# Optimization experiments

Hardware: AMD Instinct MI355X
Metric: run time of the kernel (lower is better)

## Reference

```python
import jax, jax.numpy as jnp
import numpy as np

B, T, H, W, C = 4, 16, 56, 56, 128
NH = 4                       # num heads
HD = C // NH                 # head dim = 32
WS = (2, 7, 7)               # window shape (divides T,H,W -> no padding/bounding)
SS = (1, 3, 3)               # shift shape
N = WS[0] * WS[1] * WS[2]    # 98 tokens per window
L = (T // WS[0]) * (H // WS[1]) * (W // WS[2])  # 512 windows per sample
M = (2 * WS[0] - 1) * (2 * WS[1] - 1) * (2 * WS[2] - 1)  # 507 rel-pos entries
SCALE = HD ** -0.5
MLP_H = 4 * C


def _window_partition(x):
    b = x.shape[0]
    x = x.reshape(b, T // WS[0], WS[0], H // WS[1], WS[1], W // WS[2], WS[2], C)
    return x.transpose(0, 1, 3, 5, 2, 4, 6, 7).reshape(-1, N, C)


def _window_unpartition(win, b):
    x = win.reshape(b, T // WS[0], H // WS[1], W // WS[2], WS[0], WS[1], WS[2], C)
    return x.transpose(0, 1, 4, 2, 5, 3, 6, 7).reshape(b, T, H, W, C)


def _compute_mask():
    img = np.zeros((1, T, H, W, 1), dtype=np.float32)
    cnt = 0
    for ts in (slice(0, -WS[0]), slice(-WS[0], -SS[0]), slice(-SS[0], None)):
        for hs in (slice(0, -WS[1]), slice(-WS[1], -SS[1]), slice(-SS[1], None)):
            for ws in (slice(0, -WS[2]), slice(-WS[2], -SS[2]), slice(-SS[2], None)):
                img[:, ts, hs, ws, :] = cnt
                cnt += 1
    x = img.reshape(1, T // WS[0], WS[0], H // WS[1], WS[1], W // WS[2], WS[2], 1)
    mw = x.transpose(0, 1, 3, 5, 2, 4, 6, 7).reshape(-1, N)  # [L, N]
    am = mw[:, None, :] - mw[:, :, None]
    return np.where(am != 0, np.float32(-100.0), np.float32(0.0))


def _rel_pos_idx():
    coords = np.stack(np.meshgrid(np.arange(WS[0]), np.arange(WS[1]), np.arange(WS[2]), indexing='ij'))
    rel = coords.reshape(3, -1, 1) - coords.reshape(3, 1, -1)
    rel[0] += WS[0] - 1; rel[1] += WS[1] - 1; rel[2] += WS[2] - 1
    rel[0] *= (2 * WS[1] - 1) * (2 * WS[2] - 1)
    rel[1] *= 2 * WS[2] - 1
    return rel.sum(0).astype(np.int32)  # [N, N]


def _ln(x, g, b, eps=1e-5):
    mu = jnp.mean(x, axis=-1, keepdims=True)
    var = jnp.var(x, axis=-1, keepdims=True)
    return (x - mu) * jax.lax.rsqrt(var + eps) * g + b


def setup_inputs() -> dict:
    key = jax.random.key(0)
    ks = jax.random.split(key, 8)
    s = 0.02
    return {
        'x': jax.random.normal(ks[0], (B, T, H, W, C), jnp.float32),
        'g1': jnp.ones((C,), jnp.float32), 'b1': jnp.zeros((C,), jnp.float32),
        'w_qkv': jax.random.normal(ks[1], (C, 3 * C), jnp.float32) * s,
        'b_qkv': jnp.zeros((3 * C,), jnp.float32),
        'rel_pos_embed': jax.random.normal(ks[2], (NH, M), jnp.float32) * s,
        'w_proj': jax.random.normal(ks[3], (C, C), jnp.float32) * s,
        'b_proj': jnp.zeros((C,), jnp.float32),
        'g2': jnp.ones((C,), jnp.float32), 'b2': jnp.zeros((C,), jnp.float32),
        'w_fc1': jax.random.normal(ks[4], (C, MLP_H), jnp.float32) * s,
        'b_fc1': jnp.zeros((MLP_H,), jnp.float32),
        'w_fc2': jax.random.normal(ks[5], (MLP_H, C), jnp.float32) * s,
        'b_fc2': jnp.zeros((C,), jnp.float32),
        'attn_mask': jnp.asarray(_compute_mask()),      # [L, N, N]
        'rel_pos_idx': jnp.asarray(_rel_pos_idx()),     # [N, N] int32
    }


def reference(x, g1, b1, w_qkv, b_qkv, rel_pos_embed, w_proj, b_proj,
              g2, b2, w_fc1, b_fc1, w_fc2, b_fc2, attn_mask, rel_pos_idx):
    shortcut = x
    xn = _ln(x, g1, b1)
    # cyclic shift (shifted-window branch)
    sx = jnp.roll(xn, shift=(-SS[0], -SS[1], -SS[2]), axis=(1, 2, 3))
    win = _window_partition(sx)                         # [B*L, N, C]
    Bw = win.shape[0]
    qkv = (win @ w_qkv + b_qkv).reshape(Bw, N, 3, NH, HD).transpose(2, 0, 3, 1, 4)
    q, k, v = qkv[0] * SCALE, qkv[1], qkv[2]            # [Bw, NH, N, HD]
    attn = jnp.einsum('bhnd,bhmd->bhnm', q, k)          # [Bw, NH, N, N]
    bias = rel_pos_embed[:, rel_pos_idx.reshape(-1)].reshape(NH, N, N)
    attn = attn + bias[None]
    attn = attn.reshape(Bw // L, L, NH, N, N) + attn_mask[None, :, None]
    attn = jax.nn.softmax(attn.reshape(Bw, NH, N, N), axis=-1)
    out = jnp.einsum('bhnm,bhmd->bhnd', attn, v).transpose(0, 2, 1, 3).reshape(Bw, N, C)
    out = out @ w_proj + b_proj
    sx = _window_unpartition(out, x.shape[0])
    x2 = jnp.roll(sx, shift=SS, axis=(1, 2, 3))         # reverse shift
    x = shortcut + x2
    h = _ln(x, g2, b2)
    h = jax.nn.gelu(h @ w_fc1 + b_fc1, approximate=False)
    return x + (h @ w_fc2 + b_fc2)
```

## Files before the change

### kernel.cpp

```cpp
#include <hip/hip_runtime.h>
#include <hip/hip_bf16.h>
#include <cstdint>
#include <cstddef>

using bf16 = __hip_bfloat16;
typedef __attribute__((ext_vector_type(8))) short s8v;
typedef __attribute__((ext_vector_type(4))) float f4v;
typedef __attribute__((ext_vector_type(4))) unsigned short u16x4;

#define TT 16
#define HH 56
#define WWD 56
#define CC 128
#define NTOK 98
#define NWIN 2048
#define TOKENS 200704
#define MLPH 512
#define SCALEQ 0.17677669529663689f
#define NELEM 25690112LL

#define WS_WPT 49152
#define WS_W1T 65536
#define WS_W2T 131072
#define WS_RPE 196608
#define WS_BYTES 397280

__device__ __forceinline__ float bfu(unsigned short u) {
    return __uint_as_float(((unsigned int)u) << 16);
}
__device__ __forceinline__ unsigned short f2bu(float f) {
    bf16 h = __float2bfloat16(f);
    return *reinterpret_cast<unsigned short*>(&h);
}

__device__ __forceinline__ bool disc_f32(const void* g) {
    return *(const unsigned int*)g == 0x3F800000u;
}

template<bool F32> __device__ __forceinline__ float ldg(const void* p, size_t i) {
    if constexpr (F32) return ((const float*)p)[i];
    else return bfu(((const unsigned short*)p)[i]);
}
template<bool F32> __device__ __forceinline__ void stg(void* p, size_t i, float v) {
    if constexpr (F32) ((float*)p)[i] = v;
    else ((unsigned short*)p)[i] = f2bu(v);
}
template<bool F32> __device__ __forceinline__ unsigned short ldraw(const void* p, size_t i) {
    if constexpr (F32) return f2bu(((const float*)p)[i]);
    else return ((const unsigned short*)p)[i];
}
__device__ __forceinline__ unsigned short ldraw_rt(bool f32, const void* p, size_t i) {
    return f32 ? f2bu(((const float*)p)[i]) : ((const unsigned short*)p)[i];
}

__device__ __forceinline__ size_t shifted_offset(int bid) {
    int bw = bid / NTOK, n = bid - bw * NTOK;
    int b = bw >> 9, lw = bw & 511;
    int tw = lw >> 6, hw = (lw >> 3) & 7, ww = lw & 7;
    int t0 = n / 49; int r = n - t0 * 49; int h0 = r / 7; int w0 = r - h0 * 7;
    int ts = (tw * 2 + t0 + 1) & 15;
    int hs = hw * 7 + h0 + 3; if (hs >= HH) hs -= HH;
    int ws = ww * 7 + w0 + 3; if (ws >= WWD) ws -= WWD;
    return (size_t)(((b * TT + ts) * HH + hs) * WWD + ws) * CC;
}

__global__ __launch_bounds__(256) void k_prep_rt(const void* __restrict__ wq,
                                                 const void* __restrict__ wp,
                                                 const void* __restrict__ w1,
                                                 const void* __restrict__ w2,
                                                 const void* __restrict__ rpe,
                                                 unsigned short* __restrict__ ws,
                                                 int f32i) {
    bool f32 = (f32i != 0);
    int bid = blockIdx.x, t = threadIdx.x;
    if (bid == 48) {
        for (int u = t; u < 2032; u += 256)
            ws[WS_RPE + u] = (u < 2028) ? ldraw_rt(f32, rpe, u) : (unsigned short)0;
        return;
    }
    const void* src; unsigned short* dst; int R, C, tr, tc;
    if (bid < 12)      { src = wq; dst = ws;          R = 128; C = 384; tr = bid / 6;        tc = bid % 6; }
    else if (bid < 16) { src = wp; dst = ws + WS_WPT; R = 128; C = 128; tr = (bid - 12) / 2; tc = (bid - 12) & 1; }
    else if (bid < 32) { src = w1; dst = ws + WS_W1T; R = 128; C = 512; tr = (bid - 16) / 8; tc = (bid - 16) & 7; }
    else               { src = w2; dst = ws + WS_W2T; R = 512; C = 128; tr = (bid - 32) / 2; tc = (bid - 32) & 1; }
    __shared__ unsigned short tile[64][65];
    int ty = t >> 6, tx = t & 63;
#pragma unroll
    for (int k = 0; k < 16; ++k) {
        int row = k * 4 + ty;
        tile[row][tx] = ldraw_rt(f32, src, (size_t)(tr * 64 + row) * C + tc * 64 + tx);
    }
    __syncthreads();
#pragma unroll
    for (int k = 0; k < 16; ++k) {
        int col = k * 4 + ty;
        dst[(size_t)(tc * 64 + col) * R + tr * 64 + tx] = tile[tx][col];
    }
}

template<bool F32>
__global__ __launch_bounds__(256) void k_prep(const void* __restrict__ wq,
                                              const void* __restrict__ wp,
                                              const void* __restrict__ w1,
                                              const void* __restrict__ w2,
                                              const void* __restrict__ rpe,
                                              unsigned short* __restrict__ ws,
                                              const void* __restrict__ disc) {
    if (disc_f32(disc) != F32) return;
    int bid = blockIdx.x, t = threadIdx.x;
    if (bid == 48) {
        for (int u = t; u < 2032; u += 256)
            ws[WS_RPE + u] = (u < 2028) ? ldraw<F32>(rpe, u) : (unsigned short)0;
        return;
    }
    const void* src; unsigned short* dst; int R, C, tr, tc;
    if (bid < 12)      { src = wq; dst = ws;          R = 128; C = 384; tr = bid / 6;        tc = bid % 6; }
    else if (bid < 16) { src = wp; dst = ws + WS_WPT; R = 128; C = 128; tr = (bid - 12) / 2; tc = (bid - 12) & 1; }
    else if (bid < 32) { src = w1; dst = ws + WS_W1T; R = 128; C = 512; tr = (bid - 16) / 8; tc = (bid - 16) & 7; }
    else               { src = w2; dst = ws + WS_W2T; R = 512; C = 128; tr = (bid - 32) / 2; tc = (bid - 32) & 1; }
    __shared__ unsigned short tile[64][65];
    int ty = t >> 6, tx = t & 63;
#pragma unroll
    for (int k = 0; k < 16; ++k) {
        int row = k * 4 + ty;
        tile[row][tx] = ldraw<F32>(src, (size_t)(tr * 64 + row) * C + tc * 64 + tx);
    }
    __syncthreads();
#pragma unroll
    for (int k = 0; k < 16; ++k) {
        int col = k * 4 + ty;
        dst[(size_t)(tc * 64 + col) * R + tr * 64 + tx] = tile[tx][col];
    }
}

template<bool F32, bool PREP>
__global__ __launch_bounds__(256) void k_attn(const void* __restrict__ x,
                                              const void* __restrict__ g1,
                                              const void* __restrict__ b1,
                                              void* __restrict__ buf,
                                              const unsigned short* __restrict__ wsW,
                                              const void* __restrict__ bq,
                                              const void* __restrict__ wqRaw,
                                              const void* __restrict__ rpeRaw) {
    if (disc_f32(g1) != F32) return;
    __shared__ __align__(16) char smem[27552];
    int* off_i            = (int*)smem;
    int* info             = (int*)(smem + 448);
    unsigned short* xw    = (unsigned short*)(smem + 896);
    unsigned short* rpeh  = (unsigned short*)(smem + 896);
    unsigned short* Qh    = (unsigned short*)(smem + 1920);
    unsigned short* Kh    = (unsigned short*)(smem + 9760);
    unsigned short* VT    = (unsigned short*)(smem + 17600);

    int bw = blockIdx.x, lw = bw & 511, t = threadIdx.x;
    int wv = t >> 6, ln = t & 63;
    int qd = ln >> 4, lm = ln & 15;
    unsigned short* Stw = Qh + wv * 16 * 40;

    if (t < 112) {
        if (t < 98) {
            off_i[t] = (int)shifted_offset(bw * NTOK + t);
            int t0 = t / 49, r = t - t0 * 49, h0 = r / 7, w0 = r - h0 * 7;
            int tw = lw >> 6, hw = (lw >> 3) & 7, ww = lw & 7;
            int rt = (tw < 7) ? 0 : (t0 == 0 ? 1 : 2);
            int rh = (hw < 7) ? 0 : (h0 < 4 ? 1 : 2);
            int rw = (ww < 7) ? 0 : (w0 < 4 ? 1 : 2);
            info[t] = (t0 * 169 + h0 * 13 + w0) | (((rt * 3 + rh) * 3 + rw) << 10);
        } else {
            info[t] = 0;
        }
    }
    __syncthreads();

    for (int i = wv; i < 98; i += 4) {
        size_t off = (size_t)off_i[i];
        float v0 = ldg<F32>(x, off + ln), v1 = ldg<F32>(x, off + 64 + ln);
        float sm = v0 + v1, ss = v0 * v0 + v1 * v1;
#pragma unroll
        for (int o = 32; o > 0; o >>= 1) { sm += __shfl_xor(sm, o); ss += __shfl_xor(ss, o); }
        float mu = sm * (1.f / CC);
        float rstd = rsqrtf(ss * (1.f / CC) - mu * mu + 1e-5f);
        xw[i * 136 + ln]      = f2bu((v0 - mu) * rstd * ldg<F32>(g1, ln) + ldg<F32>(b1, ln));
        xw[i * 136 + 64 + ln] = f2bu((v1 - mu) * rstd * ldg<F32>(g1, ln + 64) + ldg<F32>(b1, ln + 64));
    }
    __syncthreads();

    s8v aF[2][4];
#pragma unroll
    for (int mi = 0; mi < 2; ++mi) {
        int m = wv + 4 * mi;
        int arow = (m <= 6) ? (m * 16 + lm) : 97;
        if (arow > 97) arow = 97;
#pragma unroll
        for (int ks = 0; ks < 4; ++ks)
            aF[mi][ks] = *(const s8v*)(xw + arow * 136 + ks * 32 + qd * 8);
    }
    __syncthreads();

    for (int i = t; i < 32 * 38; i += 256) VT[(i / 38) * 136 + 98 + (i % 38)] = 0;

    for (int h = 0; h < 4; ++h) {
        for (int u = t; u < 507; u += 256) {
            if constexpr (PREP) rpeh[u] = wsW[WS_RPE + h * 507 + u];
            else                rpeh[u] = ldraw<F32>(rpeRaw, h * 507 + u);
        }
        for (int g = 0; g < 6; ++g) {
            int seg = g >> 1;
            int gcol = seg * CC + h * 32 + (g & 1) * 16 + lm;
            s8v bfr[4];
            if constexpr (PREP) {
                const unsigned short* wc = wsW + (size_t)gcol * 128;
#pragma unroll
                for (int ks = 0; ks < 4; ++ks) bfr[ks] = *(const s8v*)(wc + ks * 32 + qd * 8);
            } else {
#pragma unroll
                for (int ks = 0; ks < 4; ++ks)
#pragma unroll
                    for (int j = 0; j < 8; ++j)
                        bfr[ks][j] = (short)ldraw<F32>(wqRaw, (size_t)(ks * 32 + qd * 8 + j) * 384 + gcol);
            }
            float bias = ldg<F32>(bq, gcol);
#pragma unroll
            for (int mi = 0; mi < 2; ++mi) {
                int m = wv + 4 * mi;
                if (m > 6) break;
                f4v acc = {0.f, 0.f, 0.f, 0.f};
#pragma unroll
                for (int ks = 0; ks < 4; ++ks)
                    acc = __builtin_amdgcn_mfma_f32_16x16x32_bf16(aF[mi][ks], bfr[ks], acc, 0, 0, 0);
#pragma unroll
                for (int ii = 0; ii < 4; ++ii) {
                    int tok = m * 16 + qd * 4 + ii;
                    if (tok < 98) {
                        unsigned short val = f2bu(acc[ii] + bias);
                        int dim = (g & 1) * 16 + lm;
                        if (seg == 0)      Qh[tok * 40 + dim] = val;
                        else if (seg == 1) Kh[tok * 40 + dim] = val;
                        else               VT[dim * 136 + tok] = val;
                    }
                }
            }
        }
        __syncthreads();

        for (int m = wv; m <= 6; m += 4) {
            int aci[4], idi[4];
#pragma unroll
            for (int ii = 0; ii < 4; ++ii) {
                int iw = info[m * 16 + qd * 4 + ii];
                aci[ii] = (iw & 1023) + 253;
                idi[ii] = iw >> 10;
            }
            int qrow = m * 16 + lm; if (qrow > 97) qrow = 97;
            s8v qf = *(const s8v*)(Qh + qrow * 40 + qd * 8);
            float v[7][4];
#pragma unroll
            for (int n = 0; n < 7; ++n) {
                int krow = n * 16 + lm; if (krow > 97) krow = 97;
                const s8v* bp = (const s8v*)(Kh + krow * 40 + qd * 8);
                f4v acc = {0.f, 0.f, 0.f, 0.f};
                acc = __builtin_amdgcn_mfma_f32_16x16x32_bf16(qf, *bp, acc, 0, 0, 0);
                int cj = info[n * 16 + lm];
                int aj = cj & 1023, idj = cj >> 10;
#pragma unroll
                for (int ii = 0; ii < 4; ++ii) {
                    int ti = m * 16 + qd * 4 + ii, tj = n * 16 + lm;
                    float biasv = bfu(rpeh[aci[ii] - aj]);
                    float maskv = (idi[ii] == idj) ? 0.f : -100.f;
                    v[n][ii] = (ti < 98 && tj < 98)
                        ? acc[ii] * SCALEQ + biasv + maskv : -1e30f;
                }
            }
#pragma unroll
            for (int ii = 0; ii < 4; ++ii) {
                float mx = v[0][ii];
#pragma unroll
                for (int n = 1; n < 7; ++n) mx = fmaxf(mx, v[n][ii]);
#pragma unroll
                for (int o = 8; o > 0; o >>= 1) mx = fmaxf(mx, __shfl_xor(mx, o));
                float sum = 0.f;
#pragma unroll
                for (int n = 0; n < 7; ++n) { float e = __expf(v[n][ii] - mx); v[n][ii] = e; sum += e; }
#pragma unroll
                for (int o = 8; o > 0; o >>= 1) sum += __shfl_xor(sum, o);
                float inv = 1.f / sum;
#pragma unroll
                for (int n = 0; n < 7; ++n) v[n][ii] *= inv;
            }
            f4v a0 = {0.f, 0.f, 0.f, 0.f}, a1 = {0.f, 0.f, 0.f, 0.f};
#pragma unroll
            for (int pair = 0; pair < 4; ++pair) {
                int n0 = pair * 2, n1 = pair * 2 + 1;
#pragma unroll
                for (int ii = 0; ii < 4; ++ii) {
                    Stw[(qd * 4 + ii) * 40 + lm]      = f2bu(v[n0][ii]);
                    Stw[(qd * 4 + ii) * 40 + 16 + lm] = (n1 < 7) ? f2bu(v[n1][ii]) : (unsigned short)0;
                }
                asm volatile("s_waitcnt lgkmcnt(0)" ::: "memory");
                const s8v* pa = (const s8v*)(Stw + lm * 40 + qd * 8);
                const s8v* pb0 = (const s8v*)(VT + lm * 136 + pair * 32 + qd * 8);
                const s8v* pb1 = (const s8v*)(VT + (16 + lm) * 136 + pair * 32 + qd * 8);
                a0 = __builtin_amdgcn_mfma_f32_16x16x32_bf16(*pa, *pb0, a0, 0, 0, 0);
                a1 = __builtin_amdgcn_mfma_f32_16x16x32_bf16(*pa, *pb1, a1, 0, 0, 0);
            }
#pragma unroll
            for (int ii = 0; ii < 4; ++ii) {
                int tok = m * 16 + qd * 4 + ii;
                if (tok < 98) {
                    stg<F32>(buf, (size_t)off_i[tok] + h * 32 + lm, a0[ii]);
                    stg<F32>(buf, (size_t)off_i[tok] + h * 32 + 16 + lm, a1[ii]);
                }
            }
        }
        __syncthreads();
    }
}

template<bool F32, bool PREP>
__global__ __launch_bounds__(256, 2) void k_pm(void* __restrict__ buf,
                                               const void* __restrict__ x,
                                               const unsigned short* __restrict__ wsW,
                                               const void* __restrict__ bpj,
                                               const void* __restrict__ g2,
                                               const void* __restrict__ b2,
                                               const void* __restrict__ bb1,
                                               const void* __restrict__ bb2,
                                               const void* __restrict__ disc,
                                               const void* __restrict__ wpRaw,
                                               const void* __restrict__ w1Raw,
                                               const void* __restrict__ w2Raw) {
    if (disc_f32(disc) != F32) return;
    __shared__ __align__(16) char smem[68608];
    unsigned short* Abf = (unsigned short*)smem;
    float* A32          = (float*)(smem + 17408);
    unsigned short* Hs  = (unsigned short*)(smem + 51200);
    int t = threadIdx.x, wv = t >> 6, ln = t & 63;
    int qd = ln >> 4, lm = ln & 15;
    size_t base = (size_t)blockIdx.x * 64;

    if constexpr (F32) {
        const f4v* src = (const f4v*)((const float*)buf + base * CC);
        for (int i = t * 4; i < 64 * 128; i += 1024) {
            f4v v = src[i >> 2];
            int row = i >> 7, c = i & 127;
            u16x4 pk;
#pragma unroll
            for (int j = 0; j < 4; ++j) pk[j] = f2bu(v[j]);
            *(u16x4*)(&Abf[row * 136 + c]) = pk;
        }
    } else {
        const s8v* src = (const s8v*)((const unsigned short*)buf + base * CC);
        for (int i = t * 8; i < 64 * 128; i += 2048) {
            s8v v = src[i >> 3];
            int row = i >> 7, c = i & 127;
            *(s8v*)(&Abf[row * 136 + c]) = v;
        }
    }
    __syncthreads();

    {
        s8v wpF[2][4]; float biasp[2];
#pragma unroll
        for (int gg = 0; gg < 2; ++gg) {
            int col = (wv + 4 * gg) * 16 + lm;
            if constexpr (PREP) {
                const unsigned short* wc = wsW + WS_WPT + (size_t)col * 128;
#pragma unroll
                for (int ks = 0; ks < 4; ++ks) wpF[gg][ks] = *(const s8v*)(wc + ks * 32 + qd * 8);
            } else {
#pragma unroll
                for (int ks = 0; ks < 4; ++ks)
#pragma unroll
                    for (int j = 0; j < 8; ++j)
                        wpF[gg][ks][j] = (short)ldraw<F32>(wpRaw, (size_t)(ks * 32 + qd * 8 + j) * 128 + col);
            }
            biasp[gg] = ldg<F32>(bpj, col);
        }
#pragma unroll
        for (int m = 0; m < 4; ++m) {
            s8v aF[4];
#pragma unroll
            for (int ks = 0; ks < 4; ++ks)
                aF[ks] = *(const s8v*)(Abf + (m * 16 + lm) * 136 + ks * 32 + qd * 8);
#pragma unroll
            for (int gg = 0; gg < 2; ++gg) {
                int col = (wv + 4 * gg) * 16 + lm;
                f4v acc = {0.f, 0.f, 0.f, 0.f};
#pragma unroll
                for (int ks = 0; ks < 4; ++ks)
                    acc = __builtin_amdgcn_mfma_f32_16x16x32_bf16(aF[ks], wpF[gg][ks], acc, 0, 0, 0);
#pragma unroll
                for (int ii = 0; ii < 4; ++ii) {
                    int row = m * 16 + qd * 4 + ii;
                    A32[row * 132 + col] = acc[ii] + biasp[gg] + ldg<F32>(x, (base + row) * CC + col);
                }
            }
        }
    }
    __syncthreads();

#pragma unroll
    for (int r = 0; r < 16; ++r) {
        int row = wv + 4 * r;
        float v0 = A32[row * 132 + ln], v1 = A32[row * 132 + 64 + ln];
        float sm = v0 + v1, ss = v0 * v0 + v1 * v1;
#pragma unroll
        for (int o = 32; o > 0; o >>= 1) { sm += __shfl_xor(sm, o); ss += __shfl_xor(ss, o); }
        float mu = sm * (1.f / CC);
        float rstd = rsqrtf(ss * (1.f / CC) - mu * mu + 1e-5f);
        Abf[row * 136 + ln]      = f2bu((v0 - mu) * rstd * ldg<F32>(g2, ln) + ldg<F32>(b2, ln));
        Abf[row * 136 + 64 + ln] = f2bu((v1 - mu) * rstd * ldg<F32>(g2, ln + 64) + ldg<F32>(b2, ln + 64));
    }
    __syncthreads();

    s8v aFrag[4][4];
#pragma unroll
    for (int m = 0; m < 4; ++m)
#pragma unroll
        for (int ks = 0; ks < 4; ++ks)
            aFrag[m][ks] = *(const s8v*)(Abf + (m * 16 + lm) * 136 + ks * 32 + qd * 8);

    f4v acc2[2][4];
#pragma unroll
    for (int gg = 0; gg < 2; ++gg)
#pragma unroll
        for (int m = 0; m < 4; ++m) acc2[gg][m] = {0.f, 0.f, 0.f, 0.f};

    for (int q = 0; q < 4; ++q) {
#pragma unroll
        for (int gg = 0; gg < 2; ++gg) {
            int colL = (wv + 4 * gg) * 16 + lm;
            int colG = q * 128 + colL;
            s8v bfr[4];
            if constexpr (PREP) {
                const unsigned short* wc = wsW + WS_W1T + (size_t)colG * 128;
#pragma unroll
                for (int ks = 0; ks < 4; ++ks) bfr[ks] = *(const s8v*)(wc + ks * 32 + qd * 8);
            } else {
#pragma unroll
                for (int ks = 0; ks < 4; ++ks)
#pragma unroll
                    for (int j = 0; j < 8; ++j)
                        bfr[ks][j] = (short)ldraw<F32>(w1Raw, (size_t)(ks * 32 + qd * 8 + j) * MLPH + colG);
            }
            float bias = ldg<F32>(bb1, colG);
#pragma unroll
            for (int m = 0; m < 4; ++m) {
                f4v acc = {0.f, 0.f, 0.f, 0.f};
#pragma unroll
                for (int ks = 0; ks < 4; ++ks)
                    acc = __builtin_amdgcn_mfma_f32_16x16x32_bf16(aFrag[m][ks], bfr[ks], acc, 0, 0, 0);
#pragma unroll
                for (int ii = 0; ii < 4; ++ii) {
                    int row = m * 16 + qd * 4 + ii;
                    float hv = acc[ii] + bias;
                    Hs[row * 136 + colL] = f2bu(0.5f * hv * (1.f + erff(hv * 0.70710678118654752f)));
                }
            }
        }
        s8v w2f[2][4];
#pragma unroll
        for (int gg = 0; gg < 2; ++gg) {
            int col = (wv * 2 + gg) * 16 + lm;
            if constexpr (PREP) {
                const unsigned short* wc = wsW + WS_W2T + (size_t)col * 512 + q * 128;
#pragma unroll
                for (int ksl = 0; ksl < 4; ++ksl) w2f[gg][ksl] = *(const s8v*)(wc + ksl * 32 + qd * 8);
            } else {
#pragma unroll
                for (int ksl = 0; ksl < 4; ++ksl)
#pragma unroll
                    for (int j = 0; j < 8; ++j)
                        w2f[gg][ksl][j] = (short)ldraw<F32>(w2Raw, (size_t)(q * 128 + ksl * 32 + qd * 8 + j) * CC + col);
            }
        }
        __syncthreads();
#pragma unroll
        for (int m = 0; m < 4; ++m) {
            s8v hF[4];
#pragma unroll
            for (int ksl = 0; ksl < 4; ++ksl)
                hF[ksl] = *(const s8v*)(Hs + (m * 16 + lm) * 136 + ksl * 32 + qd * 8);
#pragma unroll
            for (int gg = 0; gg < 2; ++gg)
#pragma unroll
                for (int ksl = 0; ksl < 4; ++ksl)
                    acc2[gg][m] = __builtin_amdgcn_mfma_f32_16x16x32_bf16(hF[ksl], w2f[gg][ksl], acc2[gg][m], 0, 0, 0);
        }
        __syncthreads();
    }

#pragma unroll
    for (int gg = 0; gg < 2; ++gg) {
        int col = (wv * 2 + gg) * 16 + lm;
        float bias = ldg<F32>(bb2, col);
#pragma unroll
        for (int m = 0; m < 4; ++m) {
#pragma unroll
            for (int ii = 0; ii < 4; ++ii) {
                int row = m * 16 + qd * 4 + ii;
                stg<F32>(buf, (base + row) * CC + col,
                         acc2[gg][m][ii] + bias + A32[row * 132 + col]);
            }
        }
    }
}

extern "C" void kernel_launch(void* const* d_in, const int* in_sizes, int n_in,
                              void* d_out, int out_size, void* d_ws, size_t ws_size,
                              hipStream_t stream) {
    const void* x    = d_in[0];
    const void* g1   = d_in[1];
    const void* b1   = d_in[2];
    const void* wqkv = d_in[3];
    const void* bqkv = d_in[4];
    const void* rpe  = d_in[5];
    const void* wp   = d_in[6];
    const void* bp   = d_in[7];
    const void* g2   = d_in[8];
    const void* b2   = d_in[9];
    const void* w1   = d_in[10];
    const void* bb1  = d_in[11];
    const void* w2   = d_in[12];
    const void* bb2  = d_in[13];
    void* buf = d_out;
    unsigned short* wsW = (unsigned short*)d_ws;

    bool use_ws = (d_ws != nullptr) && (ws_size >= (size_t)WS_BYTES);

    long long xb = (long long)in_sizes[0];
    bool known_f32  = (xb == NELEM * 4);
    bool known_bf16 = (xb == NELEM * 2);

    if (use_ws && (known_f32 || known_bf16)) {
        k_prep_rt<<<49, 256, 0, stream>>>(wqkv, wp, w1, w2, rpe, wsW, known_f32 ? 1 : 0);
        if (known_f32) {
            k_attn<true, true><<<NWIN, 256, 0, stream>>>(x, g1, b1, buf, wsW, bqkv, wqkv, rpe);
            k_pm<true, true><<<TOKENS / 64, 256, 0, stream>>>(buf, x, wsW, bp, g2, b2, bb1, bb2, g1, wp, w1, w2);
        } else {
            k_attn<false, true><<<NWIN, 256, 0, stream>>>(x, g1, b1, buf, wsW, bqkv, wqkv, rpe);
            k_pm<false, true><<<TOKENS / 64, 256, 0, stream>>>(buf, x, wsW, bp, g2, b2, bb1, bb2, g1, wp, w1, w2);
        }
        return;
    }

    if (use_ws) {
        k_prep<false><<<49, 256, 0, stream>>>(wqkv, wp, w1, w2, rpe, wsW, g1);
        k_prep<true> <<<49, 256, 0, stream>>>(wqkv, wp, w1, w2, rpe, wsW, g1);
        k_attn<false, true><<<NWIN, 256, 0, stream>>>(x, g1, b1, buf, wsW, bqkv, wqkv, rpe);
        k_attn<true,  true><<<NWIN, 256, 0, stream>>>(x, g1, b1, buf, wsW, bqkv, wqkv, rpe);
        k_pm<false, true><<<TOKENS / 64, 256, 0, stream>>>(buf, x, wsW, bp, g2, b2, bb1, bb2, g1, wp, w1, w2);
        k_pm<true,  true><<<TOKENS / 64, 256, 0, stream>>>(buf, x, wsW, bp, g2, b2, bb1, bb2, g1, wp, w1, w2);
    } else if (known_f32 || known_bf16) {
        if (known_f32) {
            k_attn<true, false><<<NWIN, 256, 0, stream>>>(x, g1, b1, buf, wsW, bqkv, wqkv, rpe);
            k_pm<true, false><<<TOKENS / 64, 256, 0, stream>>>(buf, x, wsW, bp, g2, b2, bb1, bb2, g1, wp, w1, w2);
        } else {
            k_attn<false, false><<<NWIN, 256, 0, stream>>>(x, g1, b1, buf, wsW, bqkv, wqkv, rpe);
            k_pm<false, false><<<TOKENS / 64, 256, 0, stream>>>(buf, x, wsW, bp, g2, b2, bb1, bb2, g1, wp, w1, w2);
        }
    } else {
        k_attn<false, false><<<NWIN, 256, 0, stream>>>(x, g1, b1, buf, wsW, bqkv, wqkv, rpe);
        k_attn<true,  false><<<NWIN, 256, 0, stream>>>(x, g1, b1, buf, wsW, bqkv, wqkv, rpe);
        k_pm<false, false><<<TOKENS / 64, 256, 0, stream>>>(buf, x, wsW, bp, g2, b2, bb1, bb2, g1, wp, w1, w2);
        k_pm<true,  false><<<TOKENS / 64, 256, 0, stream>>>(buf, x, wsW, bp, g2, b2, bb1, bb2, g1, wp, w1, w2);
    }
}
```

Baseline: 569.4 us.

## Prefetch next fc1 weight chunk and stage residual x into LDS with input

The residual x tile is now loaded in the same coalesced vectorized pass as the attention output and written straight into the fp32 LDS buffer. This replaces the scattered per-element global reads of x in the projection epilogue. The fc1 weight fragments for the next 128-column chunk are prefetched into registers before the barrier, so their load latency overlaps the fc2 MFMA work, and the loop is fully unrolled. The cost is higher register pressure from the double-buffered weight fragments, which may lower occupancy.

```diff
diff --git a/kernel.cpp b/kernel.cpp
--- a/kernel.cpp
+++ b/kernel.cpp
@@ -339,21 +339,34 @@
     size_t base = (size_t)blockIdx.x * 64;
 
     if constexpr (F32) {
-        const f4v* src = (const f4v*)((const float*)buf + base * CC);
+        const f4v* srcb = (const f4v*)((const float*)buf + base * CC);
+        const f4v* srcx = (const f4v*)((const float*)x + base * CC);
         for (int i = t * 4; i < 64 * 128; i += 1024) {
-            f4v v = src[i >> 2];
+            f4v v = srcb[i >> 2];
+            f4v xv = srcx[i >> 2];
             int row = i >> 7, c = i & 127;
             u16x4 pk;
 #pragma unroll
             for (int j = 0; j < 4; ++j) pk[j] = f2bu(v[j]);
             *(u16x4*)(&Abf[row * 136 + c]) = pk;
+            *(f4v*)(&A32[row * 132 + c]) = xv;
         }
     } else {
-        const s8v* src = (const s8v*)((const unsigned short*)buf + base * CC);
+        const s8v* srcb = (const s8v*)((const unsigned short*)buf + base * CC);
+        const s8v* srcx = (const s8v*)((const unsigned short*)x + base * CC);
         for (int i = t * 8; i < 64 * 128; i += 2048) {
-            s8v v = src[i >> 3];
+            s8v v = srcb[i >> 3];
+            s8v xv = srcx[i >> 3];
             int row = i >> 7, c = i & 127;
             *(s8v*)(&Abf[row * 136 + c]) = v;
+            f4v x0, x1;
+#pragma unroll
+            for (int j = 0; j < 4; ++j) {
+                x0[j] = bfu((unsigned short)xv[j]);
+                x1[j] = bfu((unsigned short)xv[j + 4]);
+            }
+            *(f4v*)(&A32[row * 132 + c])     = x0;
+            *(f4v*)(&A32[row * 132 + c + 4]) = x1;
         }
     }
     __syncthreads();
@@ -392,7 +405,7 @@
 #pragma unroll
                 for (int ii = 0; ii < 4; ++ii) {
                     int row = m * 16 + qd * 4 + ii;
-                    A32[row * 132 + col] = acc[ii] + biasp[gg] + ldg<F32>(x, (base + row) * CC + col);
+                    A32[row * 132 + col] += acc[ii] + biasp[gg];
                 }
             }
         }
@@ -426,34 +439,48 @@
 #pragma unroll
         for (int m = 0; m < 4; ++m) acc2[gg][m] = {0.f, 0.f, 0.f, 0.f};
 
+#define LOADW1(Q, W, B)                                                          \
+    {                                                                            \
+        _Pragma("unroll")                                                        \
+        for (int gg = 0; gg < 2; ++gg) {                                         \
+            int colL = (wv + 4 * gg) * 16 + lm;                                  \
+            int colG = (Q) * 128 + colL;                                         \
+            if constexpr (PREP) {                                                \
+                const unsigned short* wc = wsW + WS_W1T + (size_t)colG * 128;    \
+                _Pragma("unroll")                                                \
+                for (int ks = 0; ks < 4; ++ks)                                   \
+                    W[gg][ks] = *(const s8v*)(wc + ks * 32 + qd * 8);            \
+            } else {                                                             \
+                _Pragma("unroll")                                                \
+                for (int ks = 0; ks < 4; ++ks)                                   \
+                    _Pragma("unroll")                                            \
+                    for (int j = 0; j < 8; ++j)                                  \
+                        W[gg][ks][j] = (short)ldraw<F32>(w1Raw,                  \
+                            (size_t)(ks * 32 + qd * 8 + j) * MLPH + colG);       \
+            }                                                                    \
+            B[gg] = ldg<F32>(bb1, colG);                                         \
+        }                                                                        \
+    }
+
+    s8v w1A[2][4], w1B[2][4];
+    float b1A[2], b1B[2];
+    LOADW1(0, w1A, b1A);
+
+#pragma unroll
     for (int q = 0; q < 4; ++q) {
 #pragma unroll
         for (int gg = 0; gg < 2; ++gg) {
             int colL = (wv + 4 * gg) * 16 + lm;
-            int colG = q * 128 + colL;
-            s8v bfr[4];
-            if constexpr (PREP) {
-                const unsigned short* wc = wsW + WS_W1T + (size_t)colG * 128;
-#pragma unroll
-                for (int ks = 0; ks < 4; ++ks) bfr[ks] = *(const s8v*)(wc + ks * 32 + qd * 8);
-            } else {
-#pragma unroll
-                for (int ks = 0; ks < 4; ++ks)
-#pragma unroll
-                    for (int j = 0; j < 8; ++j)
-                        bfr[ks][j] = (short)ldraw<F32>(w1Raw, (size_t)(ks * 32 + qd * 8 + j) * MLPH + colG);
-            }
-            float bias = ldg<F32>(bb1, colG);
 #pragma unroll
             for (int m = 0; m < 4; ++m) {
                 f4v acc = {0.f, 0.f, 0.f, 0.f};
 #pragma unroll
                 for (int ks = 0; ks < 4; ++ks)
-                    acc = __builtin_amdgcn_mfma_f32_16x16x32_bf16(aFrag[m][ks], bfr[ks], acc, 0, 0, 0);
+                    acc = __builtin_amdgcn_mfma_f32_16x16x32_bf16(aFrag[m][ks], w1A[gg][ks], acc, 0, 0, 0);
 #pragma unroll
                 for (int ii = 0; ii < 4; ++ii) {
                     int row = m * 16 + qd * 4 + ii;
-                    float hv = acc[ii] + bias;
+                    float hv = acc[ii] + b1A[gg];
                     Hs[row * 136 + colL] = f2bu(0.5f * hv * (1.f + erff(hv * 0.70710678118654752f)));
                 }
             }
@@ -474,6 +501,7 @@
                         w2f[gg][ksl][j] = (short)ldraw<F32>(w2Raw, (size_t)(q * 128 + ksl * 32 + qd * 8 + j) * CC + col);
             }
         }
+        if (q < 3) LOADW1(q + 1, w1B, b1B);
         __syncthreads();
 #pragma unroll
         for (int m = 0; m < 4; ++m) {
@@ -488,7 +516,16 @@
                     acc2[gg][m] = __builtin_amdgcn_mfma_f32_16x16x32_bf16(hF[ksl], w2f[gg][ksl], acc2[gg][m], 0, 0, 0);
         }
         __syncthreads();
-    }
+        if (q < 3) {
+#pragma unroll
+            for (int gg = 0; gg < 2; ++gg) {
+#pragma unroll
+                for (int ks = 0; ks < 4; ++ks) w1A[gg][ks] = w1B[gg][ks];
+                b1A[gg] = b1B[gg];
+            }
+        }
+    }
+#undef LOADW1
 
 #pragma unroll
     for (int gg = 0; gg < 2; ++gg) {
```

New measurement: 557.7 us. 2.1% less time.
